# Kernel tuning notes

Measured on AMD Instinct MI355X. Metric: run time of the kernel, lower is better.

The kernel has to match this reference:

```python
import jax, jax.numpy as jnp
import numpy as np

B, H, W, C = 64, 56, 56, 192
HEADS = 6
WIN = (7, 7)
SHIFT = (3, 3)
N = WIN[0] * WIN[1]  # tokens per window = 49
EPS = 1e-5


def _rel_pos_index(ws):
    # standard Swin relative position index, shape (N, N), values in [0, (2wh-1)(2ww-1))
    coords = np.stack(np.meshgrid(np.arange(ws[0]), np.arange(ws[1]), indexing='ij'))
    cf = coords.reshape(2, -1)
    rel = (cf[:, :, None] - cf[:, None, :]).transpose(1, 2, 0)  # N,N,2
    rel[..., 0] += ws[0] - 1
    rel[..., 1] += ws[1] - 1
    rel[..., 0] *= 2 * ws[1] - 1
    return rel.sum(-1)


def _swin_attn_mask(h, w, ws, ss):
    # cyclic-shift attention mask, shape (nW, N, N), values {0, -100}
    img = np.zeros((h, w), dtype=np.float32)
    cnt = 0
    for hs in (slice(0, -ws[0]), slice(-ws[0], -ss[0]), slice(-ss[0], None)):
        for wsl in (slice(0, -ws[1]), slice(-ws[1], -ss[1]), slice(-ss[1], None)):
            img[hs, wsl] = cnt
            cnt += 1
    m = img.reshape(h // ws[0], ws[0], w // ws[1], ws[1]).transpose(0, 2, 1, 3).reshape(-1, N)
    am = m[:, None, :] - m[:, :, None]
    return np.where(am != 0, -100.0, 0.0).astype(np.float32)


def setup_inputs() -> dict:
    key = jax.random.key(0)
    ks = jax.random.split(key, 5)
    x = jax.random.normal(ks[0], (B, H, W, C), dtype=jnp.float32)
    mask_matrix = jnp.asarray(_swin_attn_mask(H, W, WIN, SHIFT))
    gamma = jnp.ones((C,), jnp.float32)
    beta = jnp.zeros((C,), jnp.float32)
    w_qkv = jax.random.normal(ks[1], (C, 3 * C), jnp.float32) * 0.02
    b_qkv = jnp.zeros((3 * C,), jnp.float32)
    rel_table = jax.random.normal(ks[2], ((2 * WIN[0] - 1) * (2 * WIN[1] - 1), HEADS), jnp.float32) * 0.02
    w_proj = jax.random.normal(ks[3], (C, C), jnp.float32) * 0.02
    b_proj = jnp.zeros((C,), jnp.float32)
    return {"x": x, "gamma": gamma, "beta": beta, "w_qkv": w_qkv, "b_qkv": b_qkv,
            "rel_table": rel_table, "w_proj": w_proj, "b_proj": b_proj,
            "mask_matrix": mask_matrix}


def reference(x, gamma, beta, w_qkv, b_qkv, rel_table, w_proj, b_proj, mask_matrix):
    b, h, w, c = x.shape
    hd = c // HEADS
    scale = hd ** -0.5

    # norm1 (LayerNorm over channels)
    mu = jnp.mean(x, axis=-1, keepdims=True)
    var = jnp.var(x, axis=-1, keepdims=True)
    x = (x - mu) * jax.lax.rsqrt(var + EPS) * gamma + beta

    # cyclic shift (H,W divisible by window -> no padding)
    sx = jnp.roll(x, shift=(-SHIFT[0], -SHIFT[1]), axis=(1, 2))

    # window partition -> (B*nW, N, C)
    nh, nw = h // WIN[0], w // WIN[1]
    win = sx.reshape(b, nh, WIN[0], nw, WIN[1], c).transpose(0, 1, 3, 2, 4, 5)
    win = win.reshape(-1, N, c)

    # window attention with relative position bias + shift mask
    qkv = (win @ w_qkv + b_qkv).reshape(-1, N, 3, HEADS, hd).transpose(2, 0, 3, 1, 4)
    q, k, v = qkv[0], qkv[1], qkv[2]  # (B_, heads, N, hd)
    attn = jnp.einsum('bhnd,bhmd->bhnm', q * scale, k)
    rpi = _rel_pos_index(WIN)
    bias = rel_table[rpi.reshape(-1)].reshape(N, N, HEADS).transpose(2, 0, 1)  # heads,N,N
    attn = attn + bias[None]
    nW = mask_matrix.shape[0]
    attn = attn.reshape(b, nW, HEADS, N, N) + mask_matrix[None, :, None]
    attn = jax.nn.softmax(attn.reshape(-1, HEADS, N, N), axis=-1)
    out = jnp.einsum('bhnm,bhmd->bhnd', attn, v).transpose(0, 2, 1, 3).reshape(-1, N, c)
    out = out @ w_proj + b_proj

    # window reverse -> (B,H,W,C)
    out = out.reshape(b, nh, nw, WIN[0], WIN[1], c).transpose(0, 1, 3, 2, 4, 5).reshape(b, h, w, c)

    # reverse cyclic shift
    return jnp.roll(out, shift=(SHIFT[0], SHIFT[1]), axis=(1, 2))
```

## Files before the change

kernel.cpp:

```cpp
#include <hip/hip_runtime.h>
#include <hip/hip_bf16.h>
#include <math.h>

typedef __bf16 bf16;
typedef __bf16 bf16x4 __attribute__((ext_vector_type(4)));
typedef __bf16 bf16x8 __attribute__((ext_vector_type(8)));
typedef float f32x4 __attribute__((ext_vector_type(4)));
typedef unsigned int u32x4 __attribute__((ext_vector_type(4)));

#define NHEADS 6
#define CDIM 192
#define IMG 56
#define NTOK 49
#define SHIFTV 3
#define XSTR 200
#define VSTR 72
#define LOG2E 1.4426950408889634f
#define SCALE 0.17677669529663687f
#define MSKNEG (-100.0f * LOG2E)

static __device__ __forceinline__ unsigned pack2bf(float lo, float hi) {
    unsigned short a = __builtin_bit_cast(unsigned short, (bf16)lo);
    unsigned short b = __builtin_bit_cast(unsigned short, (bf16)hi);
    return (unsigned)a | ((unsigned)b << 16);
}

__global__ void prep_weights(const float* __restrict__ w_qkv, const float* __restrict__ w_proj,
                             bf16* __restrict__ wqkvT, bf16* __restrict__ wprojT) {
    int i = blockIdx.x * 256 + threadIdx.x;
    if (i < 576 * 192) {
        int n = i / 192, k = i % 192;
        wqkvT[i] = (bf16)w_qkv[k * 576 + n];
    }
    if (i < 192 * 192) {
        int n = i / 192, k = i % 192;
        wprojT[i] = (bf16)w_proj[k * 192 + n];
    }
}

__global__ __launch_bounds__(512, 4) void swin_block(
    const float* __restrict__ x, const float* __restrict__ gamma, const float* __restrict__ beta,
    const bf16* __restrict__ wqkvT, const float* __restrict__ b_qkv,
    const float* __restrict__ rel_table, const bf16* __restrict__ wprojT,
    const float* __restrict__ b_proj, float* __restrict__ out)
{
    __shared__ __align__(16) bf16 BufA[64 * XSTR];
    __shared__ __align__(16) bf16 BufB[64 * XSTR];
    __shared__ __align__(16) bf16 VTs[CDIM * VSTR];
    __shared__ bf16 biasS[169 * NHEADS];

    const int blk  = blockIdx.x;
    const int bimg = blk >> 6;
    const int wy   = (blk >> 3) & 7;
    const int wx   = blk & 7;
    const int tid  = threadIdx.x;
    const int wave = tid >> 6;
    const int lane = tid & 63;

    for (int i = tid; i < 169 * NHEADS; i += 512) biasS[i] = (bf16)(rel_table[i] * LOG2E);

    {
        const float g0 = gamma[lane], g1 = gamma[lane + 64], g2 = gamma[lane + 128];
        const float b0 = beta[lane],  b1 = beta[lane + 64],  b2 = beta[lane + 128];
        for (int t = wave; t < 64; t += 8) {
            if (t < NTOK) {
                int ty = t / 7, tx = t % 7;
                int oy = wy * 7 + ty + SHIFTV; if (oy >= IMG) oy -= IMG;
                int ox = wx * 7 + tx + SHIFTV; if (ox >= IMG) ox -= IMG;
                const float* xp = x + (((size_t)bimg * IMG + oy) * IMG + ox) * CDIM;
                float v0 = xp[lane], v1 = xp[lane + 64], v2 = xp[lane + 128];
                float s = v0 + v1 + v2, ss = v0 * v0 + v1 * v1 + v2 * v2;
                #pragma unroll
                for (int off = 32; off; off >>= 1) { s += __shfl_xor(s, off); ss += __shfl_xor(ss, off); }
                float mu  = s * (1.f / 192.f);
                float var = ss * (1.f / 192.f) - mu * mu;
                float rs  = rsqrtf(var + 1e-5f);
                BufA[t * XSTR + lane      ] = (bf16)((v0 - mu) * rs * g0 + b0);
                BufA[t * XSTR + lane + 64 ] = (bf16)((v1 - mu) * rs * g1 + b1);
                BufA[t * XSTR + lane + 128] = (bf16)((v2 - mu) * rs * g2 + b2);
            } else {
                BufA[t * XSTR + lane      ] = (bf16)0.f;
                BufA[t * XSTR + lane + 64 ] = (bf16)0.f;
                BufA[t * XSTR + lane + 128] = (bf16)0.f;
            }
        }
    }
    __syncthreads();

    {
        const int lr = lane & 15, lq = lane >> 4;
        const int h0 = wave & 1;
        const int cg = wave >> 1;
        bf16x8 afrag[2][6];
        #pragma unroll
        for (int mm = 0; mm < 2; ++mm)
            #pragma unroll
            for (int k = 0; k < 6; ++k)
                afrag[mm][k] = *(const bf16x8*)&BufA[(32 * h0 + 16 * mm + lr) * XSTR + k * 32 + lq * 8];
        __syncthreads();

        for (int t = 0; t < 9; ++t) {
            const int nt = cg + 4 * t;
            const bf16* wp = wqkvT + (size_t)(nt * 16 + lr) * CDIM + lq * 8;
            bf16x8 bfrag[6];
            #pragma unroll
            for (int k = 0; k < 6; ++k) bfrag[k] = *(const bf16x8*)(wp + k * 32);
            const int sect = nt / 12;
            f32x4 acc[2];
            acc[0] = f32x4{0.f, 0.f, 0.f, 0.f}; acc[1] = f32x4{0.f, 0.f, 0.f, 0.f};
            if (sect == 2) {
                #pragma unroll
                for (int k = 0; k < 6; ++k)
                    #pragma unroll
                    for (int mm = 0; mm < 2; ++mm)
                        acc[mm] = __builtin_amdgcn_mfma_f32_16x16x32_bf16(afrag[mm][k], bfrag[k], acc[mm], 0, 0, 0);
                const int cc   = (nt - 24) * 16 + lr;
                const float bb = b_qkv[384 + cc];
                #pragma unroll
                for (int mm = 0; mm < 2; ++mm) {
                    bf16x4 v4;
                    #pragma unroll
                    for (int r = 0; r < 4; ++r) v4[r] = (bf16)(acc[mm][r] + bb);
                    *(bf16x4*)&VTs[cc * VSTR + 32 * h0 + 16 * mm + 4 * lq] = v4;
                }
            } else {
                #pragma unroll
                for (int k = 0; k < 6; ++k)
                    #pragma unroll
                    for (int mm = 0; mm < 2; ++mm)
                        acc[mm] = __builtin_amdgcn_mfma_f32_16x16x32_bf16(bfrag[k], afrag[mm][k], acc[mm], 0, 0, 0);
                const int col0 = nt * 16 + 4 * lq;
                const f32x4 bq4 = *(const f32x4*)&b_qkv[col0];
                const int ccl  = (nt % 12) * 16 + 4 * lq;
                bf16* dst = sect ? BufA : BufB;
                #pragma unroll
                for (int mm = 0; mm < 2; ++mm) {
                    bf16x4 v4;
                    #pragma unroll
                    for (int r = 0; r < 4; ++r) v4[r] = (bf16)(acc[mm][r] + bq4[r]);
                    *(bf16x4*)&dst[(32 * h0 + 16 * mm + lr) * XSTR + ccl] = v4;
                }
            }
        }
    }
    __syncthreads();

    {
        const int li = lane & 15, lq = lane >> 4;
        const int m  = wave & 3;
        const int hg = wave >> 2;
        const int i  = 16 * m + li;
        const int ic = i < NTOK ? i : NTOK - 1;
        const int iy = ic / 7, ix = ic % 7;
        const int ay = wy * 7 + iy, ax = wx * 7 + ix;
        const int ryi = (ay < 49) ? 0 : ((ay < 53) ? 1 : 2);
        const int rxi = (ax < 49) ? 0 : ((ax < 53) ? 1 : 2);
        int   rp[4][4];
        float msk[4][4];
        #pragma unroll
        for (int n = 0; n < 4; ++n)
            #pragma unroll
            for (int r = 0; r < 4; ++r) {
                int j = 16 * n + 4 * lq + r;
                if (j < NTOK) {
                    int jy = j / 7, jx = j % 7;
                    rp[n][r] = ((iy - jy + 6) * 13 + (ix - jx + 6)) * NHEADS;
                    int by = wy * 7 + jy, bx = wx * 7 + jx;
                    int ryj = (by < 49) ? 0 : ((by < 53) ? 1 : 2);
                    int rxj = (bx < 49) ? 0 : ((bx < 53) ? 1 : 2);
                    msk[n][r] = (ryi == ryj && rxi == rxj) ? 0.f : MSKNEG;
                } else { rp[n][r] = 0; msk[n][r] = -1e30f; }
            }
        const int src0 = li + 32 * (lq & 1);
        const float SC = SCALE * LOG2E;

        #pragma unroll
        for (int hh = 0; hh < 3; ++hh) {
            const int h = hg * 3 + hh;
            bf16x8 bq = *(const bf16x8*)&BufB[(16 * m + li) * XSTR + h * 32 + lq * 8];
            f32x4 st[4];
            #pragma unroll
            for (int n = 0; n < 4; ++n) {
                bf16x8 ak = *(const bf16x8*)&BufA[(16 * n + li) * XSTR + h * 32 + lq * 8];
                st[n] = __builtin_amdgcn_mfma_f32_16x16x32_bf16(ak, bq, f32x4{0.f, 0.f, 0.f, 0.f}, 0, 0, 0);
            }
            float p[4][4];
            float umax = -1e30f;
            #pragma unroll
            for (int n = 0; n < 4; ++n)
                #pragma unroll
                for (int r = 0; r < 4; ++r) {
                    float v = fmaf(st[n][r], SC, msk[n][r]) + (float)biasS[rp[n][r] + h];
                    p[n][r] = v;
                    umax = fmaxf(umax, v);
                }
            umax = fmaxf(umax, __shfl_xor(umax, 16));
            umax = fmaxf(umax, __shfl_xor(umax, 32));
            float sum = 0.f;
            #pragma unroll
            for (int n = 0; n < 4; ++n)
                #pragma unroll
                for (int r = 0; r < 4; ++r) {
                    float e = exp2f(p[n][r] - umax);
                    p[n][r] = e; sum += e;
                }
            sum += __shfl_xor(sum, 16);
            sum += __shfl_xor(sum, 32);
            const float inv = 1.f / sum;
            unsigned pk[4][2];
            #pragma unroll
            for (int n = 0; n < 4; ++n)
                #pragma unroll
                for (int s = 0; s < 2; ++s)
                    pk[n][s] = pack2bf(p[n][2 * s] * inv, p[n][2 * s + 1] * inv);
            u32x4 ptw0, ptw1;
            #pragma unroll
            for (int w = 0; w < 4; ++w) {
                int srcl = src0 + 16 * (w >> 1);
                int s = w & 1;
                unsigned a0 = (unsigned)__shfl((int)pk[0][s], srcl);
                unsigned b0 = (unsigned)__shfl((int)pk[1][s], srcl);
                unsigned a1 = (unsigned)__shfl((int)pk[2][s], srcl);
                unsigned b1 = (unsigned)__shfl((int)pk[3][s], srcl);
                ptw0[w] = (lq & 2) ? b0 : a0;
                ptw1[w] = (lq & 2) ? b1 : a1;
            }
            bf16x8 bp0 = __builtin_bit_cast(bf16x8, ptw0);
            bf16x8 bp1 = __builtin_bit_cast(bf16x8, ptw1);
            f32x4 ot[2];
            #pragma unroll
            for (int dt = 0; dt < 2; ++dt) {
                const bf16* vrow = &VTs[(h * 32 + 16 * dt + li) * VSTR + lq * 8];
                bf16x8 av0 = *(const bf16x8*)(vrow);
                bf16x8 av1 = *(const bf16x8*)(vrow + 32);
                ot[dt] = __builtin_amdgcn_mfma_f32_16x16x32_bf16(av0, bp0, f32x4{0.f, 0.f, 0.f, 0.f}, 0, 0, 0);
                ot[dt] = __builtin_amdgcn_mfma_f32_16x16x32_bf16(av1, bp1, ot[dt], 0, 0, 0);
            }
            #pragma unroll
            for (int dt = 0; dt < 2; ++dt) {
                bf16x4 o4;
                #pragma unroll
                for (int r = 0; r < 4; ++r) o4[r] = (bf16)ot[dt][r];
                *(bf16x4*)&BufB[(16 * m + li) * XSTR + h * 32 + 16 * dt + 4 * lq] = o4;
            }
        }
    }
    __syncthreads();

    {
        const int li = lane & 15, lq = lane >> 4;
        const int half = wave & 1;
        const int cg   = wave >> 1;
        bf16x8 ofrag[2][6];
        #pragma unroll
        for (int mm = 0; mm < 2; ++mm)
            #pragma unroll
            for (int k = 0; k < 6; ++k)
                ofrag[mm][k] = *(const bf16x8*)&BufB[(32 * half + 16 * mm + li) * XSTR + k * 32 + lq * 8];
        float* orow[2];
        bool   valid[2];
        #pragma unroll
        for (int mm = 0; mm < 2; ++mm) {
            const int row = 32 * half + 16 * mm + li;
            valid[mm] = row < NTOK;
            int rr = valid[mm] ? row : 0;
            int ty = rr / 7, tx = rr % 7;
            int oy = wy * 7 + ty + SHIFTV; if (oy >= IMG) oy -= IMG;
            int ox = wx * 7 + tx + SHIFTV; if (ox >= IMG) ox -= IMG;
            orow[mm] = out + (((size_t)bimg * IMG + oy) * IMG + ox) * CDIM;
        }

        for (int s3 = 0; s3 < 3; ++s3) {
            const int nt = cg + 4 * s3;
            const bf16* wp = wprojT + (size_t)(nt * 16 + li) * CDIM + lq * 8;
            bf16x8 wfrag[6];
            #pragma unroll
            for (int k = 0; k < 6; ++k) wfrag[k] = *(const bf16x8*)(wp + k * 32);
            f32x4 acc[2];
            acc[0] = f32x4{0.f, 0.f, 0.f, 0.f}; acc[1] = f32x4{0.f, 0.f, 0.f, 0.f};
            #pragma unroll
            for (int k = 0; k < 6; ++k)
                #pragma unroll
                for (int mm = 0; mm < 2; ++mm)
                    acc[mm] = __builtin_amdgcn_mfma_f32_16x16x32_bf16(wfrag[k], ofrag[mm][k], acc[mm], 0, 0, 0);
            const int c0 = nt * 16 + 4 * lq;
            const f32x4 bp = *(const f32x4*)&b_proj[c0];
            #pragma unroll
            for (int mm = 0; mm < 2; ++mm) {
                if (valid[mm]) {
                    f32x4 v;
                    #pragma unroll
                    for (int r = 0; r < 4; ++r) v[r] = acc[mm][r] + bp[r];
                    *(f32x4*)&orow[mm][c0] = v;
                }
            }
        }
    }
}

extern "C" void kernel_launch(void* const* d_in, const int* in_sizes, int n_in,
                              void* d_out, int out_size, void* d_ws, size_t ws_size,
                              hipStream_t stream) {
    const float* x           = (const float*)d_in[0];
    const float* gamma       = (const float*)d_in[1];
    const float* beta        = (const float*)d_in[2];
    const float* w_qkv       = (const float*)d_in[3];
    const float* b_qkv       = (const float*)d_in[4];
    const float* rel_table   = (const float*)d_in[5];
    const float* w_proj      = (const float*)d_in[6];
    const float* b_proj      = (const float*)d_in[7];
    float* out = (float*)d_out;

    bf16* wqkvT  = (bf16*)d_ws;
    bf16* wprojT = (bf16*)((char*)d_ws + (size_t)576 * 192 * 2);

    prep_weights<<<432, 256, 0, stream>>>(w_qkv, w_proj, wqkvT, wprojT);
    swin_block<<<4096, 512, 0, stream>>>(x, gamma, beta, wqkvT, b_qkv, rel_table,
                                         wprojT, b_proj, out);
}
```

Baseline: 361.5 us.

## Double-buffer weight fragment loads in QKV/proj GEMMs and vectorize LayerNorm loads

The QKV and projection GEMM loops are fully unrolled with two register buffers, so the global loads of the next weight tile are issued before the MFMAs on the current tile. This hides global-load latency behind matrix work. LayerNorm now handles four tokens per wave, with 16 lanes each reading 12 contiguous floats as f32x4 vectors and reducing over 16 lanes. This replaces the scalar loads and the 64-lane shuffle reduction. The extra live weight registers may increase register pressure under the 512x4 launch bounds.

```diff
diff --git a/kernel.cpp b/kernel.cpp
--- a/kernel.cpp
+++ b/kernel.cpp
@@ -19,6 +19,8 @@
 #define SCALE 0.17677669529663687f
 #define MSKNEG (-100.0f * LOG2E)
 
+#define MFMA(a, b, c) __builtin_amdgcn_mfma_f32_16x16x32_bf16(a, b, c, 0, 0, 0)
+
 static __device__ __forceinline__ unsigned pack2bf(float lo, float hi) {
     unsigned short a = __builtin_bit_cast(unsigned short, (bf16)lo);
     unsigned short b = __builtin_bit_cast(unsigned short, (bf16)hi);
@@ -56,41 +58,58 @@
     const int tid  = threadIdx.x;
     const int wave = tid >> 6;
     const int lane = tid & 63;
+    const int lr   = lane & 15;
+    const int lq   = lane >> 4;
+    const int h0   = wave & 1;
+    const int cg   = wave >> 1;
 
     for (int i = tid; i < 169 * NHEADS; i += 512) biasS[i] = (bf16)(rel_table[i] * LOG2E);
 
     {
-        const float g0 = gamma[lane], g1 = gamma[lane + 64], g2 = gamma[lane + 128];
-        const float b0 = beta[lane],  b1 = beta[lane + 64],  b2 = beta[lane + 128];
-        for (int t = wave; t < 64; t += 8) {
+        const int c0 = lr * 12;
+        const f32x4 gm0 = *(const f32x4*)&gamma[c0], gm1 = *(const f32x4*)&gamma[c0 + 4], gm2 = *(const f32x4*)&gamma[c0 + 8];
+        const f32x4 bt0 = *(const f32x4*)&beta[c0],  bt1 = *(const f32x4*)&beta[c0 + 4],  bt2 = *(const f32x4*)&beta[c0 + 8];
+        #pragma unroll
+        for (int it = 0; it < 2; ++it) {
+            const int t = it * 32 + wave * 4 + lq;
             if (t < NTOK) {
                 int ty = t / 7, tx = t % 7;
                 int oy = wy * 7 + ty + SHIFTV; if (oy >= IMG) oy -= IMG;
                 int ox = wx * 7 + tx + SHIFTV; if (ox >= IMG) ox -= IMG;
-                const float* xp = x + (((size_t)bimg * IMG + oy) * IMG + ox) * CDIM;
-                float v0 = xp[lane], v1 = xp[lane + 64], v2 = xp[lane + 128];
-                float s = v0 + v1 + v2, ss = v0 * v0 + v1 * v1 + v2 * v2;
-                #pragma unroll
-                for (int off = 32; off; off >>= 1) { s += __shfl_xor(s, off); ss += __shfl_xor(ss, off); }
+                const float* xp = x + (((size_t)bimg * IMG + oy) * IMG + ox) * CDIM + c0;
+                f32x4 v0 = *(const f32x4*)(xp), v1 = *(const f32x4*)(xp + 4), v2 = *(const f32x4*)(xp + 8);
+                float s = 0.f, ss = 0.f;
+                #pragma unroll
+                for (int r = 0; r < 4; ++r) {
+                    s  += v0[r] + v1[r] + v2[r];
+                    ss += v0[r] * v0[r] + v1[r] * v1[r] + v2[r] * v2[r];
+                }
+                #pragma unroll
+                for (int off = 1; off < 16; off <<= 1) { s += __shfl_xor(s, off); ss += __shfl_xor(ss, off); }
                 float mu  = s * (1.f / 192.f);
                 float var = ss * (1.f / 192.f) - mu * mu;
                 float rs  = rsqrtf(var + 1e-5f);
-                BufA[t * XSTR + lane      ] = (bf16)((v0 - mu) * rs * g0 + b0);
-                BufA[t * XSTR + lane + 64 ] = (bf16)((v1 - mu) * rs * g1 + b1);
-                BufA[t * XSTR + lane + 128] = (bf16)((v2 - mu) * rs * g2 + b2);
+                bf16x4 o0, o1, o2;
+                #pragma unroll
+                for (int r = 0; r < 4; ++r) {
+                    o0[r] = (bf16)((v0[r] - mu) * rs * gm0[r] + bt0[r]);
+                    o1[r] = (bf16)((v1[r] - mu) * rs * gm1[r] + bt1[r]);
+                    o2[r] = (bf16)((v2[r] - mu) * rs * gm2[r] + bt2[r]);
+                }
+                *(bf16x4*)&BufA[t * XSTR + c0    ] = o0;
+                *(bf16x4*)&BufA[t * XSTR + c0 + 4] = o1;
+                *(bf16x4*)&BufA[t * XSTR + c0 + 8] = o2;
             } else {
-                BufA[t * XSTR + lane      ] = (bf16)0.f;
-                BufA[t * XSTR + lane + 64 ] = (bf16)0.f;
-                BufA[t * XSTR + lane + 128] = (bf16)0.f;
+                bf16x4 z = {(bf16)0.f, (bf16)0.f, (bf16)0.f, (bf16)0.f};
+                *(bf16x4*)&BufA[t * XSTR + c0    ] = z;
+                *(bf16x4*)&BufA[t * XSTR + c0 + 4] = z;
+                *(bf16x4*)&BufA[t * XSTR + c0 + 8] = z;
             }
         }
     }
     __syncthreads();
 
     {
-        const int lr = lane & 15, lq = lane >> 4;
-        const int h0 = wave & 1;
-        const int cg = wave >> 1;
         bf16x8 afrag[2][6];
         #pragma unroll
         for (int mm = 0; mm < 2; ++mm)
@@ -99,57 +118,51 @@
                 afrag[mm][k] = *(const bf16x8*)&BufA[(32 * h0 + 16 * mm + lr) * XSTR + k * 32 + lq * 8];
         __syncthreads();
 
-        for (int t = 0; t < 9; ++t) {
-            const int nt = cg + 4 * t;
-            const bf16* wp = wqkvT + (size_t)(nt * 16 + lr) * CDIM + lq * 8;
-            bf16x8 bfrag[6];
-            #pragma unroll
-            for (int k = 0; k < 6; ++k) bfrag[k] = *(const bf16x8*)(wp + k * 32);
-            const int sect = nt / 12;
-            f32x4 acc[2];
-            acc[0] = f32x4{0.f, 0.f, 0.f, 0.f}; acc[1] = f32x4{0.f, 0.f, 0.f, 0.f};
-            if (sect == 2) {
-                #pragma unroll
-                for (int k = 0; k < 6; ++k)
-                    #pragma unroll
-                    for (int mm = 0; mm < 2; ++mm)
-                        acc[mm] = __builtin_amdgcn_mfma_f32_16x16x32_bf16(afrag[mm][k], bfrag[k], acc[mm], 0, 0, 0);
-                const int cc   = (nt - 24) * 16 + lr;
-                const float bb = b_qkv[384 + cc];
-                #pragma unroll
-                for (int mm = 0; mm < 2; ++mm) {
-                    bf16x4 v4;
-                    #pragma unroll
-                    for (int r = 0; r < 4; ++r) v4[r] = (bf16)(acc[mm][r] + bb);
-                    *(bf16x4*)&VTs[cc * VSTR + 32 * h0 + 16 * mm + 4 * lq] = v4;
-                }
-            } else {
-                #pragma unroll
-                for (int k = 0; k < 6; ++k)
-                    #pragma unroll
-                    for (int mm = 0; mm < 2; ++mm)
-                        acc[mm] = __builtin_amdgcn_mfma_f32_16x16x32_bf16(bfrag[k], afrag[mm][k], acc[mm], 0, 0, 0);
-                const int col0 = nt * 16 + 4 * lq;
-                const f32x4 bq4 = *(const f32x4*)&b_qkv[col0];
-                const int ccl  = (nt % 12) * 16 + 4 * lq;
-                bf16* dst = sect ? BufA : BufB;
-                #pragma unroll
-                for (int mm = 0; mm < 2; ++mm) {
-                    bf16x4 v4;
-                    #pragma unroll
-                    for (int r = 0; r < 4; ++r) v4[r] = (bf16)(acc[mm][r] + bq4[r]);
-                    *(bf16x4*)&dst[(32 * h0 + 16 * mm + lr) * XSTR + ccl] = v4;
-                }
-            }
-        }
+        const bf16* wbase = wqkvT + (size_t)lr * CDIM + lq * 8;
+#define WPTR(nt) (wbase + (size_t)(nt) * (16 * CDIM))
+#define LOADW6(dst, p) do { const bf16* _p = (p); \
+    _Pragma("unroll") for (int k = 0; k < 6; ++k) dst[k] = *(const bf16x8*)(_p + k * 32); } while (0)
+#define COMP_QK(buf, nt, dstb) do { \
+    f32x4 a0 = {0.f,0.f,0.f,0.f}, a1 = {0.f,0.f,0.f,0.f}; \
+    _Pragma("unroll") for (int k = 0; k < 6; ++k) { \
+        a0 = MFMA(buf[k], afrag[0][k], a0); \
+        a1 = MFMA(buf[k], afrag[1][k], a1); } \
+    const int ccl_ = ((nt) % 12) * 16 + 4 * lq; \
+    const f32x4 bq_ = *(const f32x4*)&b_qkv[(nt) * 16 + 4 * lq]; \
+    bf16x4 v0_, v1_; \
+    _Pragma("unroll") for (int r = 0; r < 4; ++r) { v0_[r] = (bf16)(a0[r] + bq_[r]); v1_[r] = (bf16)(a1[r] + bq_[r]); } \
+    *(bf16x4*)&dstb[(32 * h0 + lr) * XSTR + ccl_] = v0_; \
+    *(bf16x4*)&dstb[(32 * h0 + 16 + lr) * XSTR + ccl_] = v1_; } while (0)
+#define COMP_V(buf, nt) do { \
+    f32x4 a0 = {0.f,0.f,0.f,0.f}, a1 = {0.f,0.f,0.f,0.f}; \
+    _Pragma("unroll") for (int k = 0; k < 6; ++k) { \
+        a0 = MFMA(afrag[0][k], buf[k], a0); \
+        a1 = MFMA(afrag[1][k], buf[k], a1); } \
+    const int cc_ = ((nt) - 24) * 16 + lr; \
+    const float bb_ = b_qkv[384 + cc_]; \
+    bf16x4 v0_, v1_; \
+    _Pragma("unroll") for (int r = 0; r < 4; ++r) { v0_[r] = (bf16)(a0[r] + bb_); v1_[r] = (bf16)(a1[r] + bb_); } \
+    *(bf16x4*)&VTs[cc_ * VSTR + 32 * h0 + 4 * lq] = v0_; \
+    *(bf16x4*)&VTs[cc_ * VSTR + 32 * h0 + 16 + 4 * lq] = v1_; } while (0)
+
+        bf16x8 bA[6], bB[6];
+        LOADW6(bA, WPTR(cg));
+        LOADW6(bB, WPTR(cg + 4));  COMP_QK(bA, cg,      BufB);
+        LOADW6(bA, WPTR(cg + 8));  COMP_QK(bB, cg + 4,  BufB);
+        LOADW6(bB, WPTR(cg + 12)); COMP_QK(bA, cg + 8,  BufB);
+        LOADW6(bA, WPTR(cg + 16)); COMP_QK(bB, cg + 12, BufA);
+        LOADW6(bB, WPTR(cg + 20)); COMP_QK(bA, cg + 16, BufA);
+        LOADW6(bA, WPTR(cg + 24)); COMP_QK(bB, cg + 20, BufA);
+        LOADW6(bB, WPTR(cg + 28)); COMP_V (bA, cg + 24);
+        LOADW6(bA, WPTR(cg + 32)); COMP_V (bB, cg + 28);
+                                   COMP_V (bA, cg + 32);
     }
     __syncthreads();
 
     {
-        const int li = lane & 15, lq = lane >> 4;
         const int m  = wave & 3;
         const int hg = wave >> 2;
-        const int i  = 16 * m + li;
+        const int i  = 16 * m + lr;
         const int ic = i < NTOK ? i : NTOK - 1;
         const int iy = ic / 7, ix = ic % 7;
         const int ay = wy * 7 + iy, ax = wx * 7 + ix;
@@ -171,28 +184,26 @@
                     msk[n][r] = (ryi == ryj && rxi == rxj) ? 0.f : MSKNEG;
                 } else { rp[n][r] = 0; msk[n][r] = -1e30f; }
             }
-        const int src0 = li + 32 * (lq & 1);
+        const int src0 = lr + 32 * (lq & 1);
         const float SC = SCALE * LOG2E;
 
         #pragma unroll
         for (int hh = 0; hh < 3; ++hh) {
             const int h = hg * 3 + hh;
-            bf16x8 bq = *(const bf16x8*)&BufB[(16 * m + li) * XSTR + h * 32 + lq * 8];
+            bf16x8 bq = *(const bf16x8*)&BufB[(16 * m + lr) * XSTR + h * 32 + lq * 8];
             f32x4 st[4];
             #pragma unroll
             for (int n = 0; n < 4; ++n) {
-                bf16x8 ak = *(const bf16x8*)&BufA[(16 * n + li) * XSTR + h * 32 + lq * 8];
-                st[n] = __builtin_amdgcn_mfma_f32_16x16x32_bf16(ak, bq, f32x4{0.f, 0.f, 0.f, 0.f}, 0, 0, 0);
-            }
-            float p[4][4];
+                bf16x8 ak = *(const bf16x8*)&BufA[(16 * n + lr) * XSTR + h * 32 + lq * 8];
+                st[n] = MFMA(ak, bq, (f32x4{0.f, 0.f, 0.f, 0.f}));
+            }
             float umax = -1e30f;
             #pragma unroll
             for (int n = 0; n < 4; ++n)
                 #pragma unroll
                 for (int r = 0; r < 4; ++r) {
-                    float v = fmaf(st[n][r], SC, msk[n][r]) + (float)biasS[rp[n][r] + h];
-                    p[n][r] = v;
-                    umax = fmaxf(umax, v);
+                    st[n][r] = fmaf(st[n][r], SC, msk[n][r]) + (float)biasS[rp[n][r] + h];
+                    umax = fmaxf(umax, st[n][r]);
                 }
             umax = fmaxf(umax, __shfl_xor(umax, 16));
             umax = fmaxf(umax, __shfl_xor(umax, 32));
@@ -201,8 +212,8 @@
             for (int n = 0; n < 4; ++n)
                 #pragma unroll
                 for (int r = 0; r < 4; ++r) {
-                    float e = exp2f(p[n][r] - umax);
-                    p[n][r] = e; sum += e;
+                    float e = exp2f(st[n][r] - umax);
+                    st[n][r] = e; sum += e;
                 }
             sum += __shfl_xor(sum, 16);
             sum += __shfl_xor(sum, 32);
@@ -212,7 +223,7 @@
             for (int n = 0; n < 4; ++n)
                 #pragma unroll
                 for (int s = 0; s < 2; ++s)
-                    pk[n][s] = pack2bf(p[n][2 * s] * inv, p[n][2 * s + 1] * inv);
+                    pk[n][s] = pack2bf(st[n][2 * s] * inv, st[n][2 * s + 1] * inv);
             u32x4 ptw0, ptw1;
             #pragma unroll
             for (int w = 0; w < 4; ++w) {
@@ -230,38 +241,35 @@
             f32x4 ot[2];
             #pragma unroll
             for (int dt = 0; dt < 2; ++dt) {
-                const bf16* vrow = &VTs[(h * 32 + 16 * dt + li) * VSTR + lq * 8];
+                const bf16* vrow = &VTs[(h * 32 + 16 * dt + lr) * VSTR + lq * 8];
                 bf16x8 av0 = *(const bf16x8*)(vrow);
                 bf16x8 av1 = *(const bf16x8*)(vrow + 32);
-                ot[dt] = __builtin_amdgcn_mfma_f32_16x16x32_bf16(av0, bp0, f32x4{0.f, 0.f, 0.f, 0.f}, 0, 0, 0);
-                ot[dt] = __builtin_amdgcn_mfma_f32_16x16x32_bf16(av1, bp1, ot[dt], 0, 0, 0);
+                ot[dt] = MFMA(av0, bp0, (f32x4{0.f, 0.f, 0.f, 0.f}));
+                ot[dt] = MFMA(av1, bp1, ot[dt]);
             }
             #pragma unroll
             for (int dt = 0; dt < 2; ++dt) {
                 bf16x4 o4;
                 #pragma unroll
                 for (int r = 0; r < 4; ++r) o4[r] = (bf16)ot[dt][r];
-                *(bf16x4*)&BufB[(16 * m + li) * XSTR + h * 32 + 16 * dt + 4 * lq] = o4;
+                *(bf16x4*)&BufB[(16 * m + lr) * XSTR + h * 32 + 16 * dt + 4 * lq] = o4;
             }
         }
     }
     __syncthreads();
 
     {
-        const int li = lane & 15, lq = lane >> 4;
-        const int half = wave & 1;
-        const int cg   = wave >> 1;
         bf16x8 ofrag[2][6];
         #pragma unroll
         for (int mm = 0; mm < 2; ++mm)
             #pragma unroll
             for (int k = 0; k < 6; ++k)
-                ofrag[mm][k] = *(const bf16x8*)&BufB[(32 * half + 16 * mm + li) * XSTR + k * 32 + lq * 8];
+                ofrag[mm][k] = *(const bf16x8*)&BufB[(32 * h0 + 16 * mm + lr) * XSTR + k * 32 + lq * 8];
         float* orow[2];
         bool   valid[2];
         #pragma unroll
         for (int mm = 0; mm < 2; ++mm) {
-            const int row = 32 * half + 16 * mm + li;
+            const int row = 32 * h0 + 16 * mm + lr;
             valid[mm] = row < NTOK;
             int rr = valid[mm] ? row : 0;
             int ty = rr / 7, tx = rr % 7;
@@ -270,31 +278,24 @@
             orow[mm] = out + (((size_t)bimg * IMG + oy) * IMG + ox) * CDIM;
         }
 
-        for (int s3 = 0; s3 < 3; ++s3) {
-            const int nt = cg + 4 * s3;
-            const bf16* wp = wprojT + (size_t)(nt * 16 + li) * CDIM + lq * 8;
-            bf16x8 wfrag[6];
-            #pragma unroll
-            for (int k = 0; k < 6; ++k) wfrag[k] = *(const bf16x8*)(wp + k * 32);
-            f32x4 acc[2];
-            acc[0] = f32x4{0.f, 0.f, 0.f, 0.f}; acc[1] = f32x4{0.f, 0.f, 0.f, 0.f};
-            #pragma unroll
-            for (int k = 0; k < 6; ++k)
-                #pragma unroll
-                for (int mm = 0; mm < 2; ++mm)
-                    acc[mm] = __builtin_amdgcn_mfma_f32_16x16x32_bf16(wfrag[k], ofrag[mm][k], acc[mm], 0, 0, 0);
-            const int c0 = nt * 16 + 4 * lq;
-            const f32x4 bp = *(const f32x4*)&b_proj[c0];
-            #pragma unroll
-            for (int mm = 0; mm < 2; ++mm) {
-                if (valid[mm]) {
-                    f32x4 v;
-                    #pragma unroll
-                    for (int r = 0; r < 4; ++r) v[r] = acc[mm][r] + bp[r];
-                    *(f32x4*)&orow[mm][c0] = v;
-                }
-            }
-        }
+        const bf16* pbase = wprojT + (size_t)lr * CDIM + lq * 8;
+#define PPTR(nt) (pbase + (size_t)(nt) * (16 * CDIM))
+#define COMP3(buf, nt) do { \
+    f32x4 a0 = {0.f,0.f,0.f,0.f}, a1 = {0.f,0.f,0.f,0.f}; \
+    _Pragma("unroll") for (int k = 0; k < 6; ++k) { \
+        a0 = MFMA(buf[k], ofrag[0][k], a0); \
+        a1 = MFMA(buf[k], ofrag[1][k], a1); } \
+    const int c0_ = (nt) * 16 + 4 * lq; \
+    const f32x4 bp_ = *(const f32x4*)&b_proj[c0_]; \
+    if (valid[0]) { f32x4 v_; _Pragma("unroll") for (int r = 0; r < 4; ++r) v_[r] = a0[r] + bp_[r]; *(f32x4*)&orow[0][c0_] = v_; } \
+    if (valid[1]) { f32x4 v_; _Pragma("unroll") for (int r = 0; r < 4; ++r) v_[r] = a1[r] + bp_[r]; *(f32x4*)&orow[1][c0_] = v_; } \
+} while (0)
+
+        bf16x8 pA[6], pB[6];
+        LOADW6(pA, PPTR(cg));
+        LOADW6(pB, PPTR(cg + 4)); COMP3(pA, cg);
+        LOADW6(pA, PPTR(cg + 8)); COMP3(pB, cg + 4);
+                                  COMP3(pA, cg + 8);
     }
 }
 
```

After: 341.4 us. -5.6%, faster.
